# Kernel tuning notes

Hardware: AMD Instinct MI355X
Metric: run time of the kernel (lower is better)

Reference implementation:

```python
import jax, jax.numpy as jnp
import numpy as np

B, T, D, H = 2, 2048, 768, 12
DH = D // H  # 64

def setup_inputs() -> dict:
    key = jax.random.key(0)
    k1, k2, k3 = jax.random.split(key, 3)
    x = jax.random.normal(k1, (B, T, D), dtype=jnp.float32)
    W_qkv = jax.random.normal(k2, (D, 3 * D), dtype=jnp.float32) * (D ** -0.5)
    b_qkv = jax.random.normal(k3, (3 * D,), dtype=jnp.float32) * 0.02
    return {"x": x, "W_qkv": W_qkv, "b_qkv": b_qkv}

def reference(x, W_qkv, b_qkv):
    b, t, d = x.shape
    qkv = x @ W_qkv + b_qkv  # [b, t, 3*d]
    # 'b t (qkv h d) -> qkv b h t d'
    qkv = qkv.reshape(b, t, 3, H, DH).transpose(2, 0, 3, 1, 4)
    q, k, v = qkv[0], qkv[1], qkv[2]  # each [b, h, t, dh]
    scale = DH ** -0.5
    scores = jnp.einsum('bhid,bhjd->bhij', q, k) * scale  # [b, h, t, t]
    attn = jax.nn.softmax(scores, axis=-1)
    out = jnp.einsum('bhij,bhjd->bhid', attn, v)  # [b, h, t, dh]
    # 'b h t d -> b t (h d)'
    return out.transpose(0, 2, 1, 3).reshape(b, t, d)
```

## Files before the change

### kernel.cpp

```cpp
#include <hip/hip_runtime.h>
#include <hip/hip_bf16.h>
#include <stdint.h>

typedef __bf16 bf16_t;
typedef __bf16 v8bf  __attribute__((ext_vector_type(8)));
typedef __bf16 v4bf  __attribute__((ext_vector_type(4)));
typedef float  f32x4 __attribute__((ext_vector_type(4)));
typedef unsigned short u16x8 __attribute__((ext_vector_type(8)));

#define B_   2
#define T_   2048
#define D_   768
#define H_   12
#define DH_  64
#define N3_  2304
#define M_   4096

__device__ __forceinline__ void gll16(const void* g, void* l) {
  __builtin_amdgcn_global_load_lds(
      (const __attribute__((address_space(1))) void*)g,
      (__attribute__((address_space(3))) void*)l,
      16, 0, 0);
}

__device__ __forceinline__ float bf2f(unsigned short u) {
  union { unsigned u; float f; } x; x.u = ((unsigned)u) << 16; return x.f;
}

__global__ __launch_bounds__(256) void k_conv_x(const float* __restrict__ x,
                                                bf16_t* __restrict__ xb, int n4) {
  int i = blockIdx.x * 256 + threadIdx.x;
  if (i < n4) {
    float4 v = ((const float4*)x)[i];
    v4bf o = {(bf16_t)v.x, (bf16_t)v.y, (bf16_t)v.z, (bf16_t)v.w};
    *(v4bf*)(xb + (size_t)i * 4) = o;
  }
}

__global__ __launch_bounds__(256) void k_conv_wt(const float* __restrict__ W,
                                                 bf16_t* __restrict__ Wt) {
  __shared__ bf16_t tile[64 * 64];
  const int tid = threadIdx.x;
  const int n0 = blockIdx.x * 64;
  const int k0 = blockIdx.y * 64;
  #pragma unroll
  for (int rr = 0; rr < 4; ++rr) {
    int k  = rr * 16 + (tid >> 4);
    int gr = tid & 15;
    float4 v = *(const float4*)(W + (size_t)(k0 + k) * N3_ + n0 + gr * 4);
    v4bf o = {(bf16_t)v.x, (bf16_t)v.y, (bf16_t)v.z, (bf16_t)v.w};
    *(v4bf*)(tile + k * 64 + ((gr ^ (k & 15)) << 2)) = o;
  }
  __syncthreads();
  const int n = tid & 63, q = tid >> 6;
  bf16_t outv[16] __attribute__((aligned(16)));
  #pragma unroll
  for (int tt = 0; tt < 16; ++tt) {
    int k = q * 16 + tt;
    outv[tt] = tile[k * 64 + (((n >> 2) ^ (k & 15)) << 2) + (n & 3)];
  }
  bf16_t* dst = Wt + (size_t)(n0 + n) * D_ + k0 + q * 16;
  *(u16x8*)dst       = *(const u16x8*)outv;
  *((u16x8*)dst + 1) = *(const u16x8*)(outv + 8);
}

#define BK 32
__global__ __launch_bounds__(256) void k_gemm(const bf16_t* __restrict__ A,
                                              const bf16_t* __restrict__ Bt,
                                              const float*  __restrict__ bias,
                                              bf16_t* __restrict__ Cq,
                                              bf16_t* __restrict__ vt) {
  __shared__ bf16_t As[128 * BK];
  __shared__ bf16_t Bs[128 * BK];
  const int tid  = threadIdx.x;
  const int wave = tid >> 6, lane = tid & 63;
  const int g = lane >> 4, c = lane & 15;
  const int wy = wave >> 1, wx = wave & 1;
  const int bm = blockIdx.y * 128, bn = blockIdx.x * 128;

  const f32x4 zf = {0.f, 0.f, 0.f, 0.f};
  f32x4 acc[4][4];
  #pragma unroll
  for (int i = 0; i < 4; ++i)
    #pragma unroll
    for (int j = 0; j < 4; ++j) acc[i][j] = zf;

  const int rA = tid >> 2;
  const int kc = (tid & 3) * 8;

  for (int k0 = 0; k0 < D_; k0 += BK) {
    __syncthreads();
    #pragma unroll
    for (int cc = 0; cc < 2; ++cc) {
      gll16(A  + (size_t)(bm + cc * 64 + rA) * D_ + k0 + kc,
            (char*)As + cc * 4096 + wave * 1024);
      gll16(Bt + (size_t)(bn + cc * 64 + rA) * D_ + k0 + kc,
            (char*)Bs + cc * 4096 + wave * 1024);
    }
    __syncthreads();
    v8bf af[4], bfr[4];
    #pragma unroll
    for (int mi = 0; mi < 4; ++mi)
      af[mi] = *(const v8bf*)(As + (wy * 64 + mi * 16 + c) * BK + g * 8);
    #pragma unroll
    for (int ni = 0; ni < 4; ++ni)
      bfr[ni] = *(const v8bf*)(Bs + (wx * 64 + ni * 16 + c) * BK + g * 8);
    #pragma unroll
    for (int mi = 0; mi < 4; ++mi)
      #pragma unroll
      for (int ni = 0; ni < 4; ++ni)
        acc[mi][ni] = __builtin_amdgcn_mfma_f32_16x16x32_bf16(af[mi], bfr[ni], acc[mi][ni], 0, 0, 0);
  }

  if (bn >= 2 * D_) {
    const int hb = ((bn - 2 * D_) >> 6) + wx;
    #pragma unroll
    for (int ni = 0; ni < 4; ++ni) {
      float bv = bias[bn + wx * 64 + ni * 16 + c];
      const int d = ni * 16 + c;
      #pragma unroll
      for (int mi = 0; mi < 4; ++mi) {
        int row = bm + wy * 64 + mi * 16 + g * 4;
        int b = row >> 11, t = row & (T_ - 1);
        int tl = t & 63;
        int sp = (t & ~63) | (tl & 35) | ((tl & 12) << 1) | ((tl & 16) >> 2);
        v4bf o = {(bf16_t)(acc[mi][ni][0] + bv), (bf16_t)(acc[mi][ni][1] + bv),
                  (bf16_t)(acc[mi][ni][2] + bv), (bf16_t)(acc[mi][ni][3] + bv)};
        *(v4bf*)(vt + ((size_t)((b * H_ + hb) * DH_ + d)) * T_ + sp) = o;
      }
    }
  } else {
    const float qscale = (bn < D_) ? 0.18033688011112042f : 1.0f;
    #pragma unroll
    for (int ni = 0; ni < 4; ++ni) {
      float bv = bias[bn + wx * 64 + ni * 16 + c];
      #pragma unroll
      for (int mi = 0; mi < 4; ++mi) {
        int row = bm + wy * 64 + mi * 16 + g * 4;
        bf16_t* d0 = Cq + (size_t)row * N3_ + bn + wx * 64 + ni * 16 + c;
        #pragma unroll
        for (int j = 0; j < 4; ++j)
          d0[(size_t)j * N3_] = (bf16_t)((acc[mi][ni][j] + bv) * qscale);
      }
    }
  }
}

template<int SPLIT>
__global__ __launch_bounds__(256) void k_attn(const bf16_t* __restrict__ qkv,
                                              const bf16_t* __restrict__ vt,
                                              float* __restrict__ outp,
                                              float* __restrict__ lpart) {
  __shared__ __align__(16) bf16_t Ks[64 * 64];
  __shared__ __align__(16) bf16_t Vs[64 * 64];
  const int tid  = threadIdx.x;
  const int wave = tid >> 6, lane = tid & 63;
  const int g = lane >> 4, c = lane & 15;
  const int qt = blockIdx.x;
  const int bh = blockIdx.y;
  const int z  = (SPLIT == 2) ? blockIdx.z : 0;
  const int b = bh / H_, h = bh - b * H_;
  const int r0 = z * (T_ / SPLIT);

  v8bf aq[2];
  {
    const bf16_t* qb = qkv + ((size_t)(b * T_ + qt * 64 + wave * 16 + c)) * N3_ + h * DH_ + g * 8;
    aq[0] = *(const v8bf*)qb;
    aq[1] = *(const v8bf*)(qb + 32);
  }
  float lsum = 0.f;
  const f32x4 zf = {0.f, 0.f, 0.f, 0.f};
  f32x4 oacc[4];
  #pragma unroll
  for (int ni = 0; ni < 4; ++ni) oacc[ni] = zf;

  const int rS  = tid >> 3;
  const int grS = tid & 7;
  const bf16_t* gK[2];
  const bf16_t* gV[2];
  #pragma unroll
  for (int cc = 0; cc < 2; ++cc) {
    int r    = cc * 32 + rS;
    int colk = ((grS ^ (r & 7)) << 3);
    gK[cc] = qkv + ((size_t)(b * T_ + r0 + r)) * N3_ + D_ + h * DH_ + colk;
    gV[cc] = vt + ((size_t)(bh * DH_ + r)) * T_ + r0 + colk;
  }

  {
    float4 krA = *(const float4*)gK[0], krB = *(const float4*)gK[1];
    float4 vrA = *(const float4*)gV[0], vrB = *(const float4*)gV[1];
    gK[0] += 64 * (size_t)N3_;  gK[1] += 64 * (size_t)N3_;
    gV[0] += 64;                gV[1] += 64;
    ((float4*)Ks)[tid]       = krA;
    ((float4*)Ks)[tid + 256] = krB;
    ((float4*)Vs)[tid]       = vrA;
    ((float4*)Vs)[tid + 256] = vrB;
  }
  __syncthreads();

  const int NT = T_ / (64 * SPLIT);

  for (int kt = 0; kt < NT; ++kt) {
    const bool pf = (kt + 1 < NT);
    float4 krA, krB, vrA, vrB;
    if (pf) {
      krA = *(const float4*)gK[0]; krB = *(const float4*)gK[1];
      vrA = *(const float4*)gV[0]; vrB = *(const float4*)gV[1];
      gK[0] += 64 * (size_t)N3_;  gK[1] += 64 * (size_t)N3_;
      gV[0] += 64;                gV[1] += 64;
    }

    f32x4 s[4] = {zf, zf, zf, zf};
    __builtin_amdgcn_s_setprio(1);
    #pragma unroll
    for (int kk = 0; kk < 2; ++kk) {
      #pragma unroll
      for (int ni = 0; ni < 4; ++ni) {
        const int row = ni * 16 + c;
        v8bf bk = *(const v8bf*)(Ks + row * 64 + ((kk * 32 + g * 8) ^ ((row & 7) << 3)));
        s[ni] = __builtin_amdgcn_mfma_f32_16x16x32_bf16(bk, aq[kk], s[ni], 0, 0, 0);
      }
    }
    __builtin_amdgcn_s_setprio(0);

    float rsub = 0.f;
    v8bf apk[2];
    #pragma unroll
    for (int ni = 0; ni < 4; ++ni) {
      float p0 = __builtin_amdgcn_exp2f(s[ni][0]);
      float p1 = __builtin_amdgcn_exp2f(s[ni][1]);
      float p2 = __builtin_amdgcn_exp2f(s[ni][2]);
      float p3 = __builtin_amdgcn_exp2f(s[ni][3]);
      rsub += (p0 + p1) + (p2 + p3);
      const int kkh = ni >> 1, off = (ni & 1) * 4;
      apk[kkh][off + 0] = (bf16_t)p0;
      apk[kkh][off + 1] = (bf16_t)p1;
      apk[kkh][off + 2] = (bf16_t)p2;
      apk[kkh][off + 3] = (bf16_t)p3;
    }
    lsum += rsub;

    __builtin_amdgcn_s_setprio(1);
    #pragma unroll
    for (int kk = 0; kk < 2; ++kk) {
      #pragma unroll
      for (int ni = 0; ni < 4; ++ni) {
        const int row = ni * 16 + c;
        v8bf bv = *(const v8bf*)(Vs + row * 64 + ((kk * 32 + g * 8) ^ ((row & 7) << 3)));
        oacc[ni] = __builtin_amdgcn_mfma_f32_16x16x32_bf16(bv, apk[kk], oacc[ni], 0, 0, 0);
      }
    }
    __builtin_amdgcn_s_setprio(0);

    if (pf) {
      __syncthreads();
      ((float4*)Ks)[tid]       = krA;
      ((float4*)Ks)[tid + 256] = krB;
      ((float4*)Vs)[tid]       = vrA;
      ((float4*)Vs)[tid + 256] = vrB;
      __syncthreads();
    }
  }

  lsum += __shfl_xor(lsum, 16);
  lsum += __shfl_xor(lsum, 32);
  const float inv = 1.0f / lsum;
  const int q = qt * 64 + wave * 16 + c;
  if (SPLIT == 2) {
    if (g == 0) lpart[(size_t)z * (B_ * H_ * T_) + (b * H_ + h) * T_ + q] = lsum;
    bf16_t* ob = (bf16_t*)outp + ((size_t)(z * B_ * T_ + b * T_ + q)) * D_ + h * DH_;
    #pragma unroll
    for (int ni = 0; ni < 4; ++ni) {
      v4bf o4 = {(bf16_t)(oacc[ni][0] * inv), (bf16_t)(oacc[ni][1] * inv),
                 (bf16_t)(oacc[ni][2] * inv), (bf16_t)(oacc[ni][3] * inv)};
      *(v4bf*)(ob + ni * 16 + g * 4) = o4;
    }
  } else {
    float* ob = outp + ((size_t)(b * T_ + q)) * D_ + h * DH_;
    #pragma unroll
    for (int ni = 0; ni < 4; ++ni) {
      float4 o4 = {oacc[ni][0] * inv, oacc[ni][1] * inv, oacc[ni][2] * inv, oacc[ni][3] * inv};
      *(float4*)(ob + ni * 16 + g * 4) = o4;
    }
  }
}

__global__ __launch_bounds__(256) void k_combine(const bf16_t* __restrict__ op,
                                                 const float* __restrict__ lp,
                                                 float* __restrict__ out) {
  const int i = blockIdx.x * 256 + threadIdx.x;
  const int e  = i * 8;
  const int tg = e / D_;
  const int d  = e - tg * D_;
  const int h  = d >> 6;
  const int b  = tg >> 11;
  const int t  = tg & (T_ - 1);
  const int li = (b * H_ + h) * T_ + t;
  const float la = lp[li], lb = lp[B_ * H_ * T_ + li];
  const float inv = 1.0f / (la + lb);
  const float wa = la * inv, wb = lb * inv;
  u16x8 ua = *(const u16x8*)(op + e);
  u16x8 ub = *(const u16x8*)(op + (size_t)M_ * D_ + e);
  float4 o0 = {bf2f(ua[0]) * wa + bf2f(ub[0]) * wb, bf2f(ua[1]) * wa + bf2f(ub[1]) * wb,
               bf2f(ua[2]) * wa + bf2f(ub[2]) * wb, bf2f(ua[3]) * wa + bf2f(ub[3]) * wb};
  float4 o1 = {bf2f(ua[4]) * wa + bf2f(ub[4]) * wb, bf2f(ua[5]) * wa + bf2f(ub[5]) * wb,
               bf2f(ua[6]) * wa + bf2f(ub[6]) * wb, bf2f(ua[7]) * wa + bf2f(ub[7]) * wb};
  *(float4*)(out + e)     = o0;
  *(float4*)(out + e + 4) = o1;
}

extern "C" void kernel_launch(void* const* d_in, const int* in_sizes, int n_in,
                              void* d_out, int out_size, void* d_ws, size_t ws_size,
                              hipStream_t stream) {
  const float* x    = (const float*)d_in[0];
  const float* W    = (const float*)d_in[1];
  const float* bias = (const float*)d_in[2];
  float* out = (float*)d_out;
  char* ws = (char*)d_ws;
  bf16_t* xb    = (bf16_t*)(ws);
  bf16_t* wt    = (bf16_t*)(ws + 6291456);
  bf16_t* qkvb  = (bf16_t*)(ws + 9830400);
  bf16_t* vtb   = (bf16_t*)(ws + 28704768);
  bf16_t* opart = (bf16_t*)(ws + 34996224);
  float*  lpart = (float*)(ws + 47579136);
  const size_t need_split = 47972352;

  k_conv_x <<<dim3(3072),    dim3(256), 0, stream>>>(x, xb, (M_ * D_) / 4);
  k_conv_wt<<<dim3(36, 12),  dim3(256), 0, stream>>>(W, wt);
  k_gemm   <<<dim3(18, 32),  dim3(256), 0, stream>>>(xb, wt, bias, qkvb, vtb);
  if (ws_size >= need_split) {
    k_attn<2><<<dim3(32, 24, 2), dim3(256), 0, stream>>>(qkvb, vtb, (float*)opart, lpart);
    k_combine<<<dim3(1536), dim3(256), 0, stream>>>(opart, lpart, out);
  } else {
    k_attn<1><<<dim3(32, 24), dim3(256), 0, stream>>>(qkvb, vtb, out, nullptr);
  }
}
```

Before: 87.90 us.

## Load K/V MFMA fragments directly from global memory, dropping LDS staging

```diff
diff --git a/kernel.cpp b/kernel.cpp
--- a/kernel.cpp
+++ b/kernel.cpp
@@ -15,6 +15,7 @@
 #define DH_  64
 #define N3_  2304
 #define M_   4096
+#define SPLIT_ 2
 
 __device__ __forceinline__ void gll16(const void* g, void* l) {
   __builtin_amdgcn_global_load_lds(
@@ -151,14 +152,12 @@
                                               const bf16_t* __restrict__ vt,
                                               float* __restrict__ outp,
                                               float* __restrict__ lpart) {
-  __shared__ __align__(16) bf16_t Ks[64 * 64];
-  __shared__ __align__(16) bf16_t Vs[64 * 64];
   const int tid  = threadIdx.x;
   const int wave = tid >> 6, lane = tid & 63;
   const int g = lane >> 4, c = lane & 15;
   const int qt = blockIdx.x;
   const int bh = blockIdx.y;
-  const int z  = (SPLIT == 2) ? blockIdx.z : 0;
+  const int z  = (SPLIT > 1) ? blockIdx.z : 0;
   const int b = bh / H_, h = bh - b * H_;
   const int r0 = z * (T_ / SPLIT);
 
@@ -174,53 +173,32 @@
   #pragma unroll
   for (int ni = 0; ni < 4; ++ni) oacc[ni] = zf;
 
-  const int rS  = tid >> 3;
-  const int grS = tid & 7;
-  const bf16_t* gK[2];
-  const bf16_t* gV[2];
-  #pragma unroll
-  for (int cc = 0; cc < 2; ++cc) {
-    int r    = cc * 32 + rS;
-    int colk = ((grS ^ (r & 7)) << 3);
-    gK[cc] = qkv + ((size_t)(b * T_ + r0 + r)) * N3_ + D_ + h * DH_ + colk;
-    gV[cc] = vt + ((size_t)(bh * DH_ + r)) * T_ + r0 + colk;
-  }
-
-  {
-    float4 krA = *(const float4*)gK[0], krB = *(const float4*)gK[1];
-    float4 vrA = *(const float4*)gV[0], vrB = *(const float4*)gV[1];
-    gK[0] += 64 * (size_t)N3_;  gK[1] += 64 * (size_t)N3_;
-    gV[0] += 64;                gV[1] += 64;
-    ((float4*)Ks)[tid]       = krA;
-    ((float4*)Ks)[tid + 256] = krB;
-    ((float4*)Vs)[tid]       = vrA;
-    ((float4*)Vs)[tid + 256] = vrB;
-  }
-  __syncthreads();
+  const bf16_t* kb = qkv + ((size_t)(b * T_ + r0 + c)) * N3_ + D_ + h * DH_ + g * 8;
+  const bf16_t* vb = vt + ((size_t)(bh * DH_ + c)) * T_ + r0 + g * 8;
 
   const int NT = T_ / (64 * SPLIT);
-
   for (int kt = 0; kt < NT; ++kt) {
-    const bool pf = (kt + 1 < NT);
-    float4 krA, krB, vrA, vrB;
-    if (pf) {
-      krA = *(const float4*)gK[0]; krB = *(const float4*)gK[1];
-      vrA = *(const float4*)gV[0]; vrB = *(const float4*)gV[1];
-      gK[0] += 64 * (size_t)N3_;  gK[1] += 64 * (size_t)N3_;
-      gV[0] += 64;                gV[1] += 64;
-    }
+    v8bf kf[2][4], vf[2][4];
+    #pragma unroll
+    for (int kk = 0; kk < 2; ++kk)
+      #pragma unroll
+      for (int ni = 0; ni < 4; ++ni)
+        kf[kk][ni] = *(const v8bf*)(kb + (size_t)ni * 16 * N3_ + kk * 32);
+    #pragma unroll
+    for (int kk = 0; kk < 2; ++kk)
+      #pragma unroll
+      for (int ni = 0; ni < 4; ++ni)
+        vf[kk][ni] = *(const v8bf*)(vb + (size_t)ni * 16 * T_ + kk * 32);
+    kb += 64 * (size_t)N3_;
+    vb += 64;
 
     f32x4 s[4] = {zf, zf, zf, zf};
     __builtin_amdgcn_s_setprio(1);
     #pragma unroll
-    for (int kk = 0; kk < 2; ++kk) {
-      #pragma unroll
-      for (int ni = 0; ni < 4; ++ni) {
-        const int row = ni * 16 + c;
-        v8bf bk = *(const v8bf*)(Ks + row * 64 + ((kk * 32 + g * 8) ^ ((row & 7) << 3)));
-        s[ni] = __builtin_amdgcn_mfma_f32_16x16x32_bf16(bk, aq[kk], s[ni], 0, 0, 0);
-      }
-    }
+    for (int kk = 0; kk < 2; ++kk)
+      #pragma unroll
+      for (int ni = 0; ni < 4; ++ni)
+        s[ni] = __builtin_amdgcn_mfma_f32_16x16x32_bf16(kf[kk][ni], aq[kk], s[ni], 0, 0, 0);
     __builtin_amdgcn_s_setprio(0);
 
     float rsub = 0.f;
@@ -242,33 +220,20 @@
 
     __builtin_amdgcn_s_setprio(1);
     #pragma unroll
-    for (int kk = 0; kk < 2; ++kk) {
-      #pragma unroll
-      for (int ni = 0; ni < 4; ++ni) {
-        const int row = ni * 16 + c;
-        v8bf bv = *(const v8bf*)(Vs + row * 64 + ((kk * 32 + g * 8) ^ ((row & 7) << 3)));
-        oacc[ni] = __builtin_amdgcn_mfma_f32_16x16x32_bf16(bv, apk[kk], oacc[ni], 0, 0, 0);
-      }
-    }
+    for (int kk = 0; kk < 2; ++kk)
+      #pragma unroll
+      for (int ni = 0; ni < 4; ++ni)
+        oacc[ni] = __builtin_amdgcn_mfma_f32_16x16x32_bf16(vf[kk][ni], apk[kk], oacc[ni], 0, 0, 0);
     __builtin_amdgcn_s_setprio(0);
-
-    if (pf) {
-      __syncthreads();
-      ((float4*)Ks)[tid]       = krA;
-      ((float4*)Ks)[tid + 256] = krB;
-      ((float4*)Vs)[tid]       = vrA;
-      ((float4*)Vs)[tid + 256] = vrB;
-      __syncthreads();
-    }
   }
 
   lsum += __shfl_xor(lsum, 16);
   lsum += __shfl_xor(lsum, 32);
   const float inv = 1.0f / lsum;
   const int q = qt * 64 + wave * 16 + c;
-  if (SPLIT == 2) {
+  if (SPLIT > 1) {
     if (g == 0) lpart[(size_t)z * (B_ * H_ * T_) + (b * H_ + h) * T_ + q] = lsum;
-    bf16_t* ob = (bf16_t*)outp + ((size_t)(z * B_ * T_ + b * T_ + q)) * D_ + h * DH_;
+    bf16_t* ob = (bf16_t*)outp + ((size_t)z * M_ * D_ + ((size_t)(b * T_ + q)) * D_ + h * DH_);
     #pragma unroll
     for (int ni = 0; ni < 4; ++ni) {
       v4bf o4 = {(bf16_t)(oacc[ni][0] * inv), (bf16_t)(oacc[ni][1] * inv),
@@ -296,15 +261,19 @@
   const int b  = tg >> 11;
   const int t  = tg & (T_ - 1);
   const int li = (b * H_ + h) * T_ + t;
-  const float la = lp[li], lb = lp[B_ * H_ * T_ + li];
-  const float inv = 1.0f / (la + lb);
-  const float wa = la * inv, wb = lb * inv;
-  u16x8 ua = *(const u16x8*)(op + e);
-  u16x8 ub = *(const u16x8*)(op + (size_t)M_ * D_ + e);
-  float4 o0 = {bf2f(ua[0]) * wa + bf2f(ub[0]) * wb, bf2f(ua[1]) * wa + bf2f(ub[1]) * wb,
-               bf2f(ua[2]) * wa + bf2f(ub[2]) * wb, bf2f(ua[3]) * wa + bf2f(ub[3]) * wb};
-  float4 o1 = {bf2f(ua[4]) * wa + bf2f(ub[4]) * wb, bf2f(ua[5]) * wa + bf2f(ub[5]) * wb,
-               bf2f(ua[6]) * wa + bf2f(ub[6]) * wb, bf2f(ua[7]) * wa + bf2f(ub[7]) * wb};
+  float acc[8] = {0.f, 0.f, 0.f, 0.f, 0.f, 0.f, 0.f, 0.f};
+  float ltot = 0.f;
+  #pragma unroll
+  for (int z = 0; z < SPLIT_; ++z) {
+    const float lz = lp[(size_t)z * (B_ * H_ * T_) + li];
+    ltot += lz;
+    u16x8 u = *(const u16x8*)(op + (size_t)z * M_ * D_ + e);
+    #pragma unroll
+    for (int j = 0; j < 8; ++j) acc[j] += bf2f(u[j]) * lz;
+  }
+  const float inv = 1.0f / ltot;
+  float4 o0 = {acc[0] * inv, acc[1] * inv, acc[2] * inv, acc[3] * inv};
+  float4 o1 = {acc[4] * inv, acc[5] * inv, acc[6] * inv, acc[7] * inv};
   *(float4*)(out + e)     = o0;
   *(float4*)(out + e + 4) = o1;
 }
@@ -329,7 +298,7 @@
   k_conv_wt<<<dim3(36, 12),  dim3(256), 0, stream>>>(W, wt);
   k_gemm   <<<dim3(18, 32),  dim3(256), 0, stream>>>(xb, wt, bias, qkvb, vtb);
   if (ws_size >= need_split) {
-    k_attn<2><<<dim3(32, 24, 2), dim3(256), 0, stream>>>(qkvb, vtb, (float*)opart, lpart);
+    k_attn<SPLIT_><<<dim3(32, 24, SPLIT_), dim3(256), 0, stream>>>(qkvb, vtb, (float*)opart, lpart);
     k_combine<<<dim3(1536), dim3(256), 0, stream>>>(opart, lpart, out);
   } else {
     k_attn<1><<<dim3(32, 24), dim3(256), 0, stream>>>(qkvb, vtb, out, nullptr);
```

Measured after the change: 216.6 us. 146% more time.
